# Performance work log

Hardware: AMD Instinct MI355X
Metric: run time of the kernel (lower is better)

## Reference

```python
import jax, jax.numpy as jnp
import numpy as np

D_MODEL = 1024
NHEAD = 16
HEAD_DIM = D_MODEL // NHEAD
B, T = 2, 2048


def setup_inputs() -> dict:
    key = jax.random.key(0)
    ks = jax.random.split(key, 11)
    s = 1.0 / np.sqrt(D_MODEL)
    inp = {
        'q': jax.random.normal(ks[0], (B, T, D_MODEL), jnp.float32),
        'k': jax.random.normal(ks[1], (B, T, D_MODEL), jnp.float32),
        'v': jax.random.normal(ks[2], (B, T, D_MODEL), jnp.float32),
        'Wq': jax.random.normal(ks[3], (D_MODEL, D_MODEL), jnp.float32) * s,
        'bq': jnp.zeros((D_MODEL,), jnp.float32),
        'Wk': jax.random.normal(ks[4], (D_MODEL, D_MODEL), jnp.float32) * s,
        'bk': jnp.zeros((D_MODEL,), jnp.float32),
        'Wv': jax.random.normal(ks[5], (D_MODEL, D_MODEL), jnp.float32) * s,
        'bv': jnp.zeros((D_MODEL,), jnp.float32),
        'Wo': jax.random.normal(ks[6], (D_MODEL, D_MODEL), jnp.float32) * s,
        'bo': jnp.zeros((D_MODEL,), jnp.float32),
    }
    return inp


def reference(q, k, v, Wq, bq, Wk, bk, Wv, bv, Wo, bo):
    scale = np.sqrt(HEAD_DIM).astype(np.float32)
    # projections (torch Linear: x @ W.T + b), split heads -> [B, H, T, Dh]
    def proj(x, W, b):
        y = jnp.einsum('btd,ed->bte', x, W) + b
        return y.reshape(B, T, NHEAD, HEAD_DIM).transpose(0, 2, 1, 3)
    qh = proj(q, Wq, bq)
    kh = proj(k, Wk, bk)
    vh = proj(v, Wv, bv)
    scores = jnp.einsum('bhqd,bhkd->bhqk', qh, kh) / scale  # [B,H,T,T]
    weights = jax.nn.softmax(scores, axis=-1)
    out = jnp.einsum('bhqk,bhkd->bhqd', weights, vh)        # [B,H,T,Dh]
    out = out.transpose(0, 2, 1, 3).reshape(B, T, D_MODEL)
    return jnp.einsum('btd,ed->bte', out, Wo) + bo
```

## Files before the change

### kernel.cpp

```cpp
#include <hip/hip_runtime.h>
#include <cstdint>
#include <cstddef>


#define D_MODEL 1024
#define NHEAD   16
#define HDIM    64
#define BATCH   2
#define SEQ     2048
#define BT      (BATCH * SEQ)

#define QSCALE 0.18033688011112043f

typedef __bf16 bf16;
typedef __bf16 bf16x8 __attribute__((ext_vector_type(8)));
typedef __bf16 bf16x4 __attribute__((ext_vector_type(4)));
typedef float  floatx4 __attribute__((ext_vector_type(4)));
typedef short  short4v __attribute__((ext_vector_type(4)));

#define MFMA16(a, b, c) __builtin_amdgcn_mfma_f32_16x16x32_bf16((a), (b), (c), 0, 0, 0)

__device__ __forceinline__ floatx4 MFMA16B(bf16x4 a, bf16x4 b, floatx4 c) {
  return __builtin_amdgcn_mfma_f32_16x16x16bf16_1k(
      __builtin_bit_cast(short4v, a), __builtin_bit_cast(short4v, b), c, 0, 0, 0);
}

__device__ __forceinline__ float fexp2(float x) {
  return __builtin_amdgcn_exp2f(x);
}

__device__ __forceinline__ void async_cp16(const bf16* g, bf16* l) {
  __builtin_amdgcn_global_load_lds(
      (__attribute__((address_space(1))) void*)(g),
      (__attribute__((address_space(3))) void*)(l), 16, 0, 0);
}

__global__ __launch_bounds__(256) void cvt7(
    const float* __restrict__ s0, const float* __restrict__ s1,
    const float* __restrict__ s2, const float* __restrict__ s3,
    const float* __restrict__ s4, const float* __restrict__ s5,
    const float* __restrict__ s6,
    bf16* __restrict__ d0, bf16* __restrict__ d1, bf16* __restrict__ d2,
    bf16* __restrict__ d3, bf16* __restrict__ d4, bf16* __restrict__ d5,
    bf16* __restrict__ d6)
{
  const float* src; bf16* dst; int n4;
  switch (blockIdx.y) {
    case 0:  src = s0; dst = d0; n4 = (BT * D_MODEL) / 4; break;
    case 1:  src = s1; dst = d1; n4 = (BT * D_MODEL) / 4; break;
    case 2:  src = s2; dst = d2; n4 = (BT * D_MODEL) / 4; break;
    case 3:  src = s3; dst = d3; n4 = (D_MODEL * D_MODEL) / 4; break;
    case 4:  src = s4; dst = d4; n4 = (D_MODEL * D_MODEL) / 4; break;
    case 5:  src = s5; dst = d5; n4 = (D_MODEL * D_MODEL) / 4; break;
    default: src = s6; dst = d6; n4 = (D_MODEL * D_MODEL) / 4; break;
  }
  int stride = gridDim.x * blockDim.x;
  for (int i = blockIdx.x * blockDim.x + threadIdx.x; i < n4; i += stride) {
    float4 f = ((const float4*)src)[i];
    bf16x4 h;
    h[0] = (bf16)f.x; h[1] = (bf16)f.y; h[2] = (bf16)f.z; h[3] = (bf16)f.w;
    ((bf16x4*)dst)[i] = h;
  }
}

__device__ __forceinline__ void gemm128_core(
    const bf16* __restrict__ A, const bf16* __restrict__ W,
    int m0, int n0, bf16* As, bf16* Bs, floatx4 acc[4][4])
{
  const int t = threadIdx.x;
  const int l = t & 63, w = t >> 6;
  const int quad = l >> 4, lr = l & 15;
  const int wm = (w >> 1) * 64, wn = (w & 1) * 64;

  floatx4 z = {0.f, 0.f, 0.f, 0.f};
#pragma unroll
  for (int i = 0; i < 4; i++)
#pragma unroll
    for (int j = 0; j < 4; j++) acc[i][j] = z;

  for (int kt = 0; kt < 1024; kt += 32) {
    __syncthreads();
#pragma unroll
    for (int i = 0; i < 2; i++) {
      int c = i * 256 + t;
      int row = c >> 2, ci = c & 3;
      async_cp16(A + (size_t)(m0 + row) * 1024 + kt + ci * 8,
                 As + (i * 256 + w * 64) * 8);
      async_cp16(W + (size_t)(n0 + row) * 1024 + kt + ci * 8,
                 Bs + (i * 256 + w * 64) * 8);
    }
    __syncthreads();

    bf16x8 af[4], bfr[4];
#pragma unroll
    for (int i = 0; i < 4; i++) {
      af[i]  = *(const bf16x8*)(As + (wm + i * 16 + lr) * 32 + quad * 8);
      bfr[i] = *(const bf16x8*)(Bs + (wn + i * 16 + lr) * 32 + quad * 8);
    }
#pragma unroll
    for (int i = 0; i < 4; i++)
#pragma unroll
      for (int j = 0; j < 4; j++)
        acc[i][j] = MFMA16(af[i], bfr[j], acc[i][j]);
  }
}

__global__ __launch_bounds__(256) void qkv_gemm(
    const bf16* __restrict__ qb, const bf16* __restrict__ kb, const bf16* __restrict__ vb,
    const bf16* __restrict__ wq, const bf16* __restrict__ wk, const bf16* __restrict__ wv,
    const float* __restrict__ biasq, const float* __restrict__ biask, const float* __restrict__ biasv,
    bf16* __restrict__ qh, bf16* __restrict__ kh, bf16* __restrict__ vt)
{
  __shared__ bf16 As[128 * 32];
  __shared__ bf16 Bs[128 * 32];
  const int zid = blockIdx.z;
  const bf16* A = (zid == 0) ? qb : ((zid == 1) ? kb : vb);
  const bf16* W = (zid == 0) ? wq : ((zid == 1) ? wk : wv);
  const float* bias = (zid == 0) ? biasq : ((zid == 1) ? biask : biasv);
  const int m0 = blockIdx.x * 128, n0 = blockIdx.y * 128;

  floatx4 acc[4][4];
  gemm128_core(A, W, m0, n0, As, Bs, acc);

  const int t = threadIdx.x, l = t & 63, w = t >> 6;
  const int quad = l >> 4, lr = l & 15;
  const int wm = (w >> 1) * 64, wn = (w & 1) * 64;
  const float sc = (zid == 0) ? QSCALE : 1.0f;

  if (zid < 2) {
    bf16* out = (zid == 0) ? qh : kh;
#pragma unroll
    for (int i = 0; i < 4; i++) {
      int mbase = m0 + wm + i * 16 + quad * 4;
      int b  = mbase >> 11;
      int tq = mbase & 2047;
#pragma unroll
      for (int j = 0; j < 4; j++) {
        int n = n0 + wn + j * 16 + lr;
        float bv = bias[n];
        int h = n >> 6, dh = n & 63;
        bf16* p = out + ((size_t)((b * NHEAD + h) * SEQ + tq)) * HDIM + dh;
#pragma unroll
        for (int r = 0; r < 4; r++)
          p[(size_t)r * HDIM] = (bf16)((acc[i][j][r] + bv) * sc);
      }
    }
  } else {
#pragma unroll
    for (int i = 0; i < 4; i++) {
      int mbase = m0 + wm + i * 16 + quad * 4;
      int b  = mbase >> 11;
      int tq = mbase & 2047;
#pragma unroll
      for (int j = 0; j < 4; j++) {
        int n = n0 + wn + j * 16 + lr;
        float bv = bias[n];
        int h = n >> 6, dh = n & 63;
        bf16x4 pk;
#pragma unroll
        for (int r = 0; r < 4; r++) pk[r] = (bf16)(acc[i][j][r] + bv);
        *(bf16x4*)(vt + ((size_t)((b * NHEAD + h) * HDIM + dh)) * SEQ + tq) = pk;
      }
    }
  }
}

__global__ __launch_bounds__(256, 2) void attn_fused(
    const bf16* __restrict__ qh, const bf16* __restrict__ kh,
    const bf16* __restrict__ vt, bf16* __restrict__ attn)
{
  __shared__ __align__(16) char smem[65536];

  const int t = threadIdx.x, l = t & 63, w = t >> 6;
  const int quad = l >> 4, lr = l & 15;

  const int hb  = blockIdx.y * 16 + blockIdx.x;
  const int j   = hb >> 3;
  const int bh  = (hb & 7) + ((j & 3) << 3);
  const int qt0 = (j >> 2) * 128;

  const bf16* qg = qh + (size_t)bh * SEQ * HDIM;
  const bf16* kg = kh + (size_t)bh * SEQ * HDIM;
  const bf16* vg = vt + (size_t)bh * HDIM * SEQ;

  const bf16* kseg[4];
  const bf16* vseg[4];
#pragma unroll
  for (int i = 0; i < 4; i++) {
    int s = w * 4 + i;
    int krow = s * 8 + (l >> 3);
    kseg[i] = kg + (size_t)krow * HDIM + (((l & 7) ^ (l >> 3)) * 8);
    int vrow = s * 4 + (l >> 4);
    vseg[i] = vg + (size_t)vrow * SEQ + (((l & 15) ^ (vrow & 15)) * 8);
  }

  bf16x8 qf[2][2];
#pragma unroll
  for (int g = 0; g < 2; g++)
#pragma unroll
    for (int ko = 0; ko < 2; ko++)
      qf[g][ko] = *(const bf16x8*)(qg + (size_t)(qt0 + w * 32 + g * 16 + lr) * HDIM
                                   + ko * 32 + quad * 8);

  const floatx4 zz = {0.f, 0.f, 0.f, 0.f};
  floatx4 Oacc[2][4];
#pragma unroll
  for (int g = 0; g < 2; g++)
#pragma unroll
    for (int dt = 0; dt < 4; dt++) Oacc[g][dt] = zz;
  float mrow[2] = {-3.0e38f, -3.0e38f};
  float lrow[2] = {0.f, 0.f};

  auto stage = [&](int buf, int kt) {
    bf16* Kb = (bf16*)(smem + buf * 32768);
    bf16* Vb = (bf16*)(smem + buf * 32768 + 16384);
    int off = kt * 128;
#pragma unroll
    for (int i = 0; i < 4; i++) {
      async_cp16(kseg[i] + (size_t)off * HDIM, Kb + (w * 4 + i) * 512);
      async_cp16(vseg[i] + off,                Vb + (w * 4 + i) * 512);
    }
  };

  stage(0, 0);

  for (int kt = 0; kt < 16; kt++) {
    const int p = kt & 1;
    __syncthreads();
    if (kt + 1 < 16) stage(1 - p, kt + 1);
    const bf16* Ks  = (const bf16*)(smem + p * 32768);
    const bf16* Vts = (const bf16*)(smem + p * 32768 + 16384);

    const bf16* krow0 = Ks + lr * 64 + ((quad ^ (lr & 7)) * 8);
    const bf16* krow1 = Ks + lr * 64 + (((quad + 4) ^ (lr & 7)) * 8);

    floatx4 s0[8], s1[8];
#pragma unroll
    for (int ni = 0; ni < 8; ni++) {
      bf16x8 k0 = *(const bf16x8*)(krow0 + ni * 1024);
      bf16x8 k1 = *(const bf16x8*)(krow1 + ni * 1024);
      floatx4 a0 = MFMA16(k0, qf[0][0], zz);
      floatx4 a1 = MFMA16(k0, qf[1][0], zz);
      a0 = MFMA16(k1, qf[0][1], a0);
      a1 = MFMA16(k1, qf[1][1], a1);
      s0[ni] = a0;
      s1[ni] = a1;
    }

    bf16x4 pk0[8], pk1[8];
#pragma unroll
    for (int g = 0; g < 2; g++) {
      floatx4* sg = g ? s1 : s0;
      bf16x4* pkg = g ? pk1 : pk0;

      float xm[8];
#pragma unroll
      for (int ni = 0; ni < 8; ni++)
        xm[ni] = fmaxf(fmaxf(sg[ni][0], sg[ni][1]), fmaxf(sg[ni][2], sg[ni][3]));
      float rmax = fmaxf(fmaxf(fmaxf(xm[0], xm[1]), fmaxf(xm[2], xm[3])),
                         fmaxf(fmaxf(xm[4], xm[5]), fmaxf(xm[6], xm[7])));
      rmax = fmaxf(rmax, __shfl_xor(rmax, 16, 64));
      rmax = fmaxf(rmax, __shfl_xor(rmax, 32, 64));

      if (!__all(rmax - mrow[g] <= 8.0f)) {
        float mnew = fmaxf(mrow[g], rmax);
        float al = fexp2(mrow[g] - mnew);
        mrow[g] = mnew;
        lrow[g] *= al;
#pragma unroll
        for (int dt = 0; dt < 4; dt++)
#pragma unroll
          for (int r = 0; r < 4; r++) Oacc[g][dt][r] *= al;
      }

      const float m = mrow[g];
      float tt[8];
#pragma unroll
      for (int ni = 0; ni < 8; ni++) {
        float p0 = fexp2(sg[ni][0] - m), p1 = fexp2(sg[ni][1] - m);
        float p2 = fexp2(sg[ni][2] - m), p3 = fexp2(sg[ni][3] - m);
        pkg[ni][0] = (bf16)p0; pkg[ni][1] = (bf16)p1;
        pkg[ni][2] = (bf16)p2; pkg[ni][3] = (bf16)p3;
        tt[ni] = (p0 + p1) + (p2 + p3);
      }
      float rsum = ((tt[0] + tt[1]) + (tt[2] + tt[3]))
                 + ((tt[4] + tt[5]) + (tt[6] + tt[7]));
      rsum += __shfl_xor(rsum, 16, 64);
      rsum += __shfl_xor(rsum, 32, 64);
      lrow[g] += rsum;
    }

    const bf16* vbase = Vts + lr * 128 + (quad & 1) * 4;
#pragma unroll
    for (int ni = 0; ni < 8; ni++) {
      const bf16* vp = vbase + (((ni * 2 + (quad >> 1)) ^ lr) * 8);
      bf16x4 vf0 = *(const bf16x4*)(vp);
      bf16x4 vf1 = *(const bf16x4*)(vp + 2048);
      bf16x4 vf2 = *(const bf16x4*)(vp + 4096);
      bf16x4 vf3 = *(const bf16x4*)(vp + 6144);
      Oacc[0][0] = MFMA16B(vf0, pk0[ni], Oacc[0][0]);
      Oacc[1][0] = MFMA16B(vf0, pk1[ni], Oacc[1][0]);
      Oacc[0][1] = MFMA16B(vf1, pk0[ni], Oacc[0][1]);
      Oacc[1][1] = MFMA16B(vf1, pk1[ni], Oacc[1][1]);
      Oacc[0][2] = MFMA16B(vf2, pk0[ni], Oacc[0][2]);
      Oacc[1][2] = MFMA16B(vf2, pk1[ni], Oacc[1][2]);
      Oacc[0][3] = MFMA16B(vf3, pk0[ni], Oacc[0][3]);
      Oacc[1][3] = MFMA16B(vf3, pk1[ni], Oacc[1][3]);
    }
  }

  bf16* Ost = (bf16*)smem;
#pragma unroll
  for (int g = 0; g < 2; g++) {
    float inv = 1.0f / lrow[g];
#pragma unroll
    for (int dt = 0; dt < 4; dt++) {
      bf16x4 ov;
#pragma unroll
      for (int r = 0; r < 4; r++) ov[r] = (bf16)(Oacc[g][dt][r] * inv);
      *(bf16x4*)(Ost + (size_t)(w * 32 + g * 16 + lr) * 72 + dt * 16 + quad * 4) = ov;
    }
  }
  __syncthreads();

  const int b = bh >> 4, h = bh & 15;
#pragma unroll
  for (int i = 0; i < 4; i++) {
    int c = t + 256 * i;
    int row = c >> 3, ci = c & 7;
    *(int4*)(attn + ((size_t)b * SEQ + qt0 + row) * D_MODEL + h * HDIM + ci * 8) =
        *(const int4*)(Ost + row * 72 + ci * 8);
  }
}

__global__ __launch_bounds__(256) void oproj_gemm(
    const bf16* __restrict__ attn, const bf16* __restrict__ wo,
    const float* __restrict__ bo, float* __restrict__ out)
{
  __shared__ bf16 As[128 * 32];
  __shared__ bf16 Bs[64 * 32];
  const int m0 = blockIdx.x * 128, n0 = blockIdx.y * 64;
  const int t = threadIdx.x, l = t & 63, w = t >> 6;
  const int quad = l >> 4, lr = l & 15;
  const int wm = (w >> 1) * 64, wn = (w & 1) * 32;

  floatx4 z = {0.f, 0.f, 0.f, 0.f};
  floatx4 acc[4][2];
#pragma unroll
  for (int i = 0; i < 4; i++)
#pragma unroll
    for (int j = 0; j < 2; j++) acc[i][j] = z;

  for (int kt = 0; kt < 1024; kt += 32) {
    __syncthreads();
#pragma unroll
    for (int i = 0; i < 2; i++) {
      int c = i * 256 + t;
      int row = c >> 2, ci = c & 3;
      async_cp16(attn + (size_t)(m0 + row) * 1024 + kt + ci * 8,
                 As + (i * 256 + w * 64) * 8);
    }
    {
      int row = t >> 2, ci = t & 3;
      async_cp16(wo + (size_t)(n0 + row) * 1024 + kt + ci * 8,
                 Bs + (w * 64) * 8);
    }
    __syncthreads();

    bf16x8 af[4], bfr[2];
#pragma unroll
    for (int i = 0; i < 4; i++)
      af[i]  = *(const bf16x8*)(As + (wm + i * 16 + lr) * 32 + quad * 8);
#pragma unroll
    for (int j = 0; j < 2; j++)
      bfr[j] = *(const bf16x8*)(Bs + (wn + j * 16 + lr) * 32 + quad * 8);
#pragma unroll
    for (int i = 0; i < 4; i++)
#pragma unroll
      for (int j = 0; j < 2; j++)
        acc[i][j] = MFMA16(af[i], bfr[j], acc[i][j]);
  }

#pragma unroll
  for (int i = 0; i < 4; i++) {
    int m = m0 + wm + i * 16 + quad * 4;
#pragma unroll
    for (int j = 0; j < 2; j++) {
      int n = n0 + wn + j * 16 + lr;
      float bv = bo[n];
      float* p = out + (size_t)m * D_MODEL + n;
#pragma unroll
      for (int r = 0; r < 4; r++)
        p[(size_t)r * D_MODEL] = acc[i][j][r] + bv;
    }
  }
}

extern "C" void kernel_launch(void* const* d_in, const int* in_sizes, int n_in,
                              void* d_out, int out_size, void* d_ws, size_t ws_size,
                              hipStream_t stream)
{
  const float* q  = (const float*)d_in[0];
  const float* k  = (const float*)d_in[1];
  const float* v  = (const float*)d_in[2];
  const float* Wq = (const float*)d_in[3];
  const float* bq = (const float*)d_in[4];
  const float* Wk = (const float*)d_in[5];
  const float* bk = (const float*)d_in[6];
  const float* Wv = (const float*)d_in[7];
  const float* bv = (const float*)d_in[8];
  const float* Wo = (const float*)d_in[9];
  const float* bo = (const float*)d_in[10];

  const size_t NQ = (size_t)BT * D_MODEL;
  const size_t NW = (size_t)D_MODEL * D_MODEL;

  bf16* p = (bf16*)d_ws;
  bf16* qb   = p; p += NQ;
  bf16* kb   = p; p += NQ;
  bf16* vb   = p; p += NQ;
  bf16* wqb  = p; p += NW;
  bf16* wkb  = p; p += NW;
  bf16* wvb  = p; p += NW;
  bf16* wob  = p; p += NW;
  bf16* qhp  = p; p += NQ;
  bf16* khp  = p; p += NQ;
  bf16* vtp  = p; p += NQ;
  bf16* attn = p; p += NQ;

  cvt7<<<dim3(1024, 7, 1), 256, 0, stream>>>(q, k, v, Wq, Wk, Wv, Wo,
                                             qb, kb, vb, wqb, wkb, wvb, wob);
  qkv_gemm<<<dim3(32, 8, 3), 256, 0, stream>>>(qb, kb, vb, wqb, wkb, wvb,
                                               bq, bk, bv, qhp, khp, vtp);
  attn_fused<<<dim3(16, 32, 1), 256, 0, stream>>>(qhp, khp, vtp, attn);
  oproj_gemm<<<dim3(32, 16, 1), 256, 0, stream>>>(attn, wob, bo, (float*)d_out);
}
```

Before: 224.8 us.

## Fuse fp32-to-bf16 conversion into GEMM tile loads, drop separate cvt kernel

Removes the standalone cvt7 kernel that converted inputs and weights to bf16 in workspace. The QKV and output-projection GEMMs now load fp32 tiles directly from global memory, convert them in registers, and store bf16 into shared memory. This saves one launch and a full write-plus-reread of the bf16 copies. In exchange each GEMM reads twice the bytes per tile, and weight tiles are reconverted by every block that uses them. The loads are also now synchronous register round-trips instead of async global-to-LDS copies.

```diff
diff --git a/kernel.cpp b/kernel.cpp
--- a/kernel.cpp
+++ b/kernel.cpp
@@ -35,42 +35,21 @@
       (__attribute__((address_space(3))) void*)(l), 16, 0, 0);
 }
 
-__global__ __launch_bounds__(256) void cvt7(
-    const float* __restrict__ s0, const float* __restrict__ s1,
-    const float* __restrict__ s2, const float* __restrict__ s3,
-    const float* __restrict__ s4, const float* __restrict__ s5,
-    const float* __restrict__ s6,
-    bf16* __restrict__ d0, bf16* __restrict__ d1, bf16* __restrict__ d2,
-    bf16* __restrict__ d3, bf16* __restrict__ d4, bf16* __restrict__ d5,
-    bf16* __restrict__ d6)
-{
-  const float* src; bf16* dst; int n4;
-  switch (blockIdx.y) {
-    case 0:  src = s0; dst = d0; n4 = (BT * D_MODEL) / 4; break;
-    case 1:  src = s1; dst = d1; n4 = (BT * D_MODEL) / 4; break;
-    case 2:  src = s2; dst = d2; n4 = (BT * D_MODEL) / 4; break;
-    case 3:  src = s3; dst = d3; n4 = (D_MODEL * D_MODEL) / 4; break;
-    case 4:  src = s4; dst = d4; n4 = (D_MODEL * D_MODEL) / 4; break;
-    case 5:  src = s5; dst = d5; n4 = (D_MODEL * D_MODEL) / 4; break;
-    default: src = s6; dst = d6; n4 = (D_MODEL * D_MODEL) / 4; break;
-  }
-  int stride = gridDim.x * blockDim.x;
-  for (int i = blockIdx.x * blockDim.x + threadIdx.x; i < n4; i += stride) {
-    float4 f = ((const float4*)src)[i];
-    bf16x4 h;
-    h[0] = (bf16)f.x; h[1] = (bf16)f.y; h[2] = (bf16)f.z; h[3] = (bf16)f.w;
-    ((bf16x4*)dst)[i] = h;
-  }
-}
-
-__device__ __forceinline__ void gemm128_core(
-    const bf16* __restrict__ A, const bf16* __restrict__ W,
+__device__ __forceinline__ bf16x4 cvt4(float4 f) {
+  bf16x4 h;
+  h[0] = (bf16)f.x; h[1] = (bf16)f.y; h[2] = (bf16)f.z; h[3] = (bf16)f.w;
+  return h;
+}
+
+__device__ __forceinline__ void gemm128_core_f32(
+    const float* __restrict__ A, const float* __restrict__ W,
     int m0, int n0, bf16* As, bf16* Bs, floatx4 acc[4][4])
 {
   const int t = threadIdx.x;
   const int l = t & 63, w = t >> 6;
   const int quad = l >> 4, lr = l & 15;
   const int wm = (w >> 1) * 64, wn = (w & 1) * 64;
+  const int srow = t >> 3, sci = t & 7;
 
   floatx4 z = {0.f, 0.f, 0.f, 0.f};
 #pragma unroll
@@ -81,13 +60,12 @@
   for (int kt = 0; kt < 1024; kt += 32) {
     __syncthreads();
 #pragma unroll
-    for (int i = 0; i < 2; i++) {
-      int c = i * 256 + t;
-      int row = c >> 2, ci = c & 3;
-      async_cp16(A + (size_t)(m0 + row) * 1024 + kt + ci * 8,
-                 As + (i * 256 + w * 64) * 8);
-      async_cp16(W + (size_t)(n0 + row) * 1024 + kt + ci * 8,
-                 Bs + (i * 256 + w * 64) * 8);
+    for (int ii = 0; ii < 4; ii++) {
+      int row = ii * 32 + srow;
+      float4 fa = *(const float4*)(A + (size_t)(m0 + row) * 1024 + kt + sci * 4);
+      float4 fw = *(const float4*)(W + (size_t)(n0 + row) * 1024 + kt + sci * 4);
+      *(bf16x4*)(As + row * 32 + sci * 4) = cvt4(fa);
+      *(bf16x4*)(Bs + row * 32 + sci * 4) = cvt4(fw);
     }
     __syncthreads();
 
@@ -106,21 +84,21 @@
 }
 
 __global__ __launch_bounds__(256) void qkv_gemm(
-    const bf16* __restrict__ qb, const bf16* __restrict__ kb, const bf16* __restrict__ vb,
-    const bf16* __restrict__ wq, const bf16* __restrict__ wk, const bf16* __restrict__ wv,
+    const float* __restrict__ qb, const float* __restrict__ kb, const float* __restrict__ vb,
+    const float* __restrict__ wq, const float* __restrict__ wk, const float* __restrict__ wv,
     const float* __restrict__ biasq, const float* __restrict__ biask, const float* __restrict__ biasv,
     bf16* __restrict__ qh, bf16* __restrict__ kh, bf16* __restrict__ vt)
 {
   __shared__ bf16 As[128 * 32];
   __shared__ bf16 Bs[128 * 32];
   const int zid = blockIdx.z;
-  const bf16* A = (zid == 0) ? qb : ((zid == 1) ? kb : vb);
-  const bf16* W = (zid == 0) ? wq : ((zid == 1) ? wk : wv);
+  const float* A = (zid == 0) ? qb : ((zid == 1) ? kb : vb);
+  const float* W = (zid == 0) ? wq : ((zid == 1) ? wk : wv);
   const float* bias = (zid == 0) ? biasq : ((zid == 1) ? biask : biasv);
   const int m0 = blockIdx.x * 128, n0 = blockIdx.y * 128;
 
   floatx4 acc[4][4];
-  gemm128_core(A, W, m0, n0, As, Bs, acc);
+  gemm128_core_f32(A, W, m0, n0, As, Bs, acc);
 
   const int t = threadIdx.x, l = t & 63, w = t >> 6;
   const int quad = l >> 4, lr = l & 15;
@@ -334,7 +312,7 @@
 }
 
 __global__ __launch_bounds__(256) void oproj_gemm(
-    const bf16* __restrict__ attn, const bf16* __restrict__ wo,
+    const bf16* __restrict__ attn, const float* __restrict__ wo,
     const float* __restrict__ bo, float* __restrict__ out)
 {
   __shared__ bf16 As[128 * 32];
@@ -343,6 +321,7 @@
   const int t = threadIdx.x, l = t & 63, w = t >> 6;
   const int quad = l >> 4, lr = l & 15;
   const int wm = (w >> 1) * 64, wn = (w & 1) * 32;
+  const int srow = t >> 3, sci = t & 7;
 
   floatx4 z = {0.f, 0.f, 0.f, 0.f};
   floatx4 acc[4][2];
@@ -360,10 +339,11 @@
       async_cp16(attn + (size_t)(m0 + row) * 1024 + kt + ci * 8,
                  As + (i * 256 + w * 64) * 8);
     }
-    {
-      int row = t >> 2, ci = t & 3;
-      async_cp16(wo + (size_t)(n0 + row) * 1024 + kt + ci * 8,
-                 Bs + (w * 64) * 8);
+#pragma unroll
+    for (int jj = 0; jj < 2; jj++) {
+      int row = jj * 32 + srow;
+      float4 fw = *(const float4*)(wo + (size_t)(n0 + row) * 1024 + kt + sci * 4);
+      *(bf16x4*)(Bs + row * 32 + sci * 4) = cvt4(fw);
     }
     __syncthreads();
 
@@ -413,25 +393,15 @@
   const float* bo = (const float*)d_in[10];
 
   const size_t NQ = (size_t)BT * D_MODEL;
-  const size_t NW = (size_t)D_MODEL * D_MODEL;
 
   bf16* p = (bf16*)d_ws;
-  bf16* qb   = p; p += NQ;
-  bf16* kb   = p; p += NQ;
-  bf16* vb   = p; p += NQ;
-  bf16* wqb  = p; p += NW;
-  bf16* wkb  = p; p += NW;
-  bf16* wvb  = p; p += NW;
-  bf16* wob  = p; p += NW;
   bf16* qhp  = p; p += NQ;
   bf16* khp  = p; p += NQ;
   bf16* vtp  = p; p += NQ;
   bf16* attn = p; p += NQ;
 
-  cvt7<<<dim3(1024, 7, 1), 256, 0, stream>>>(q, k, v, Wq, Wk, Wv, Wo,
-                                             qb, kb, vb, wqb, wkb, wvb, wob);
-  qkv_gemm<<<dim3(32, 8, 3), 256, 0, stream>>>(qb, kb, vb, wqb, wkb, wvb,
+  qkv_gemm<<<dim3(32, 8, 3), 256, 0, stream>>>(q, k, v, Wq, Wk, Wv,
                                                bq, bk, bv, qhp, khp, vtp);
   attn_fused<<<dim3(16, 32, 1), 256, 0, stream>>>(qhp, khp, vtp, attn);
-  oproj_gemm<<<dim3(32, 16, 1), 256, 0, stream>>>(attn, wob, bo, (float*)d_out);
-}
+  oproj_gemm<<<dim3(32, 16, 1), 256, 0, stream>>>(attn, Wo, bo, (float*)d_out);
+}
```

New measurement: 242.8 us. +8.0%, slower.

## Use 16x16x32 MFMA for PV and compute row sums via MFMA with ones

Applied to the files above, without the earlier changes.

Switches the P·V product from 16x16x16 MFMAs to 16x16x32 MFMAs by packing two key tiles of P and V into bf16x8 operands, halving the MFMA instruction count. Row sums of the softmax numerator now come from an extra MFMA against a ones vector, which replaces the scalar add tree and its cross-lane shuffles. The row sum is therefore accumulated from bf16-rounded probabilities, which changes numerics slightly. The max reduction is also rewritten as a linear chain.

```diff
diff --git a/kernel.cpp b/kernel.cpp
--- a/kernel.cpp
+++ b/kernel.cpp
@@ -19,11 +19,6 @@
 typedef short  short4v __attribute__((ext_vector_type(4)));
 
 #define MFMA16(a, b, c) __builtin_amdgcn_mfma_f32_16x16x32_bf16((a), (b), (c), 0, 0, 0)
-
-__device__ __forceinline__ floatx4 MFMA16B(bf16x4 a, bf16x4 b, floatx4 c) {
-  return __builtin_amdgcn_mfma_f32_16x16x16bf16_1k(
-      __builtin_bit_cast(short4v, a), __builtin_bit_cast(short4v, b), c, 0, 0, 0);
-}
 
 __device__ __forceinline__ float fexp2(float x) {
   return __builtin_amdgcn_exp2f(x);
@@ -208,8 +203,12 @@
   for (int g = 0; g < 2; g++)
 #pragma unroll
     for (int dt = 0; dt < 4; dt++) Oacc[g][dt] = zz;
+  floatx4 Racc[2] = {zz, zz};
   float mrow[2] = {-3.0e38f, -3.0e38f};
-  float lrow[2] = {0.f, 0.f};
+
+  bf16x8 ones8;
+#pragma unroll
+  for (int i = 0; i < 8; i++) ones8[i] = (bf16)1.0f;
 
   auto stage = [&](int buf, int kt) {
     bf16* Kb = (bf16*)(smem + buf * 32768);
@@ -247,18 +246,22 @@
       s1[ni] = a1;
     }
 
-    bf16x4 pk0[8], pk1[8];
+    bf16x8 pk0[4], pk1[4];
 #pragma unroll
     for (int g = 0; g < 2; g++) {
       floatx4* sg = g ? s1 : s0;
-      bf16x4* pkg = g ? pk1 : pk0;
+      bf16x8* pkg = g ? pk1 : pk0;
 
       float xm[8];
 #pragma unroll
-      for (int ni = 0; ni < 8; ni++)
-        xm[ni] = fmaxf(fmaxf(sg[ni][0], sg[ni][1]), fmaxf(sg[ni][2], sg[ni][3]));
-      float rmax = fmaxf(fmaxf(fmaxf(xm[0], xm[1]), fmaxf(xm[2], xm[3])),
-                         fmaxf(fmaxf(xm[4], xm[5]), fmaxf(xm[6], xm[7])));
+      for (int ni = 0; ni < 8; ni++) {
+        float m01 = fmaxf(sg[ni][0], sg[ni][1]);
+        xm[ni] = fmaxf(fmaxf(m01, sg[ni][2]), sg[ni][3]);
+      }
+      float rmax = fmaxf(fmaxf(xm[0], xm[1]), xm[2]);
+      rmax = fmaxf(fmaxf(rmax, xm[3]), xm[4]);
+      rmax = fmaxf(fmaxf(rmax, xm[5]), xm[6]);
+      rmax = fmaxf(rmax, xm[7]);
       rmax = fmaxf(rmax, __shfl_xor(rmax, 16, 64));
       rmax = fmaxf(rmax, __shfl_xor(rmax, 32, 64));
 
@@ -266,53 +269,48 @@
         float mnew = fmaxf(mrow[g], rmax);
         float al = fexp2(mrow[g] - mnew);
         mrow[g] = mnew;
-        lrow[g] *= al;
 #pragma unroll
         for (int dt = 0; dt < 4; dt++)
 #pragma unroll
           for (int r = 0; r < 4; r++) Oacc[g][dt][r] *= al;
+#pragma unroll
+        for (int r = 0; r < 4; r++) Racc[g][r] *= al;
       }
 
       const float m = mrow[g];
-      float tt[8];
-#pragma unroll
-      for (int ni = 0; ni < 8; ni++) {
-        float p0 = fexp2(sg[ni][0] - m), p1 = fexp2(sg[ni][1] - m);
-        float p2 = fexp2(sg[ni][2] - m), p3 = fexp2(sg[ni][3] - m);
-        pkg[ni][0] = (bf16)p0; pkg[ni][1] = (bf16)p1;
-        pkg[ni][2] = (bf16)p2; pkg[ni][3] = (bf16)p3;
-        tt[ni] = (p0 + p1) + (p2 + p3);
-      }
-      float rsum = ((tt[0] + tt[1]) + (tt[2] + tt[3]))
-                 + ((tt[4] + tt[5]) + (tt[6] + tt[7]));
-      rsum += __shfl_xor(rsum, 16, 64);
-      rsum += __shfl_xor(rsum, 32, 64);
-      lrow[g] += rsum;
+#pragma unroll
+      for (int nip = 0; nip < 4; nip++) {
+        bf16x8 pv;
+#pragma unroll
+        for (int r = 0; r < 4; r++) pv[r]     = (bf16)fexp2(sg[2*nip  ][r] - m);
+#pragma unroll
+        for (int r = 0; r < 4; r++) pv[4 + r] = (bf16)fexp2(sg[2*nip+1][r] - m);
+        pkg[nip] = pv;
+      }
     }
 
     const bf16* vbase = Vts + lr * 128 + (quad & 1) * 4;
 #pragma unroll
-    for (int ni = 0; ni < 8; ni++) {
-      const bf16* vp = vbase + (((ni * 2 + (quad >> 1)) ^ lr) * 8);
-      bf16x4 vf0 = *(const bf16x4*)(vp);
-      bf16x4 vf1 = *(const bf16x4*)(vp + 2048);
-      bf16x4 vf2 = *(const bf16x4*)(vp + 4096);
-      bf16x4 vf3 = *(const bf16x4*)(vp + 6144);
-      Oacc[0][0] = MFMA16B(vf0, pk0[ni], Oacc[0][0]);
-      Oacc[1][0] = MFMA16B(vf0, pk1[ni], Oacc[1][0]);
-      Oacc[0][1] = MFMA16B(vf1, pk0[ni], Oacc[0][1]);
-      Oacc[1][1] = MFMA16B(vf1, pk1[ni], Oacc[1][1]);
-      Oacc[0][2] = MFMA16B(vf2, pk0[ni], Oacc[0][2]);
-      Oacc[1][2] = MFMA16B(vf2, pk1[ni], Oacc[1][2]);
-      Oacc[0][3] = MFMA16B(vf3, pk0[ni], Oacc[0][3]);
-      Oacc[1][3] = MFMA16B(vf3, pk1[ni], Oacc[1][3]);
+    for (int nip = 0; nip < 4; nip++) {
+      const bf16* vpA = vbase + ((((4 * nip)     + (quad >> 1)) ^ lr) * 8);
+      const bf16* vpB = vbase + ((((4 * nip + 2) + (quad >> 1)) ^ lr) * 8);
+      Racc[0] = MFMA16(ones8, pk0[nip], Racc[0]);
+      Racc[1] = MFMA16(ones8, pk1[nip], Racc[1]);
+#pragma unroll
+      for (int dt = 0; dt < 4; dt++) {
+        bf16x4 va = *(const bf16x4*)(vpA + dt * 2048);
+        bf16x4 vb = *(const bf16x4*)(vpB + dt * 2048);
+        bf16x8 vf8 = __builtin_shufflevector(va, vb, 0, 1, 2, 3, 4, 5, 6, 7);
+        Oacc[0][dt] = MFMA16(vf8, pk0[nip], Oacc[0][dt]);
+        Oacc[1][dt] = MFMA16(vf8, pk1[nip], Oacc[1][dt]);
+      }
     }
   }
 
   bf16* Ost = (bf16*)smem;
 #pragma unroll
   for (int g = 0; g < 2; g++) {
-    float inv = 1.0f / lrow[g];
+    float inv = 1.0f / Racc[g][0];
 #pragma unroll
     for (int dt = 0; dt < 4; dt++) {
       bf16x4 ov;
```

New measurement: 215.5 us. 4.1% less time.
